# Performance work log

Measured on AMD Instinct MI355X. Metric: run time of the kernel, lower is better.

## Reference

```python
import jax, jax.numpy as jnp
import numpy as np

N_NODES = 100_000
N_EDGES = 1_600_000
D_IN = 128
D_OUT = 128


def setup_inputs() -> dict:
    key = jax.random.key(0)
    ks = jax.random.split(key, 6)
    X = jax.random.normal(ks[0], (N_NODES, D_IN), dtype=jnp.float32)
    ref_a = jax.random.randint(ks[1], (N_EDGES,), 0, N_NODES, dtype=jnp.int64 if jax.config.jax_enable_x64 else jnp.int32)
    backref = jax.random.randint(ks[2], (N_EDGES,), 0, N_NODES, dtype=jnp.int64 if jax.config.jax_enable_x64 else jnp.int32)
    e_map = jax.random.randint(ks[3], (N_EDGES,), 0, N_NODES, dtype=jnp.int32)
    v_count = jnp.ones((1,), dtype=jnp.int32)
    # GlorotUniform init for the two projection matrices
    limit = np.sqrt(6.0 / (D_IN + D_OUT)).astype(np.float32)
    W = jax.random.uniform(ks[4], (D_IN, D_OUT), dtype=jnp.float32, minval=-limit, maxval=limit)
    W_prop = jax.random.uniform(ks[5], (D_IN, D_OUT), dtype=jnp.float32, minval=-limit, maxval=limit)
    b = jnp.zeros((D_OUT,), dtype=jnp.float32)
    return {"X": X, "ref_a": ref_a, "backref": backref, "e_map": e_map,
            "v_count": v_count, "W": W, "W_prop": W_prop, "b": b}


def reference(X, ref_a, backref, e_map, v_count, W, W_prop, b):
    # Dual linear projections
    XW = X @ W                 # [N, D_OUT]
    XW_prop = X @ W_prop       # [N, D_OUT]
    # wl1_convolution_compact: gather rows at edge sources, scatter-sum into targets
    msgs = XW_prop[ref_a]      # [E, D_OUT] irregular gather
    X_conv = jax.ops.segment_sum(msgs, backref, num_segments=X.shape[0])  # [N, D_OUT]
    # bias add + activation
    X_out = jax.nn.relu(XW + X_conv + b)
    return (X_out, ref_a, backref, e_map, v_count)
```

## Files before the change

kernel.cpp:

```cpp
#include <hip/hip_runtime.h>
#include <hip/hip_bf16.h>


#define SCAN_BE 1024

typedef __attribute__((ext_vector_type(8))) short bf16x8;
typedef __attribute__((ext_vector_type(4))) float f32x4;

__device__ __forceinline__ float bf2f(unsigned short u) {
    return __uint_as_float(((unsigned int)u) << 16);
}

__device__ __forceinline__ unsigned short f2bf(float f) {
    unsigned int b = __float_as_uint(f);
    unsigned int r = (b + 0x7FFFu + ((b >> 16) & 1u)) >> 16;
    return (unsigned short)r;
}

__device__ __forceinline__ unsigned char f2e4m3(float f) {
    unsigned int u = __float_as_uint(f);
    unsigned char s = (unsigned char)((u >> 24) & 0x80u);
    unsigned int ua = u & 0x7FFFFFFFu;
    float a = __uint_as_float(ua);
    if (!(a < 448.0f)) return (unsigned char)(s | 0x7E);
    if (a < 0x1p-10f) return s;
    int E = (int)(ua >> 23);
    int e = E - 120;
    unsigned int M = ua & 0x7FFFFFu;
    if (e >= 1) {
        unsigned int r = M + 0x7FFFFu + ((M >> 20) & 1u);
        unsigned int m = r >> 20;
        if (m >= 8) { m = 0; e++; }
        if (e >= 16 || (e == 15 && m == 7))
            return (unsigned char)(s | 0x7E);
        return (unsigned char)(s | (e << 3) | (m & 7));
    } else {
        int m = (int)(a * 512.0f + 0.5f);
        if (m >= 8) return (unsigned char)(s | 0x08);
        return (unsigned char)(s | m);
    }
}

__device__ __forceinline__ float4 load4f(const void* p, size_t off, int isbf) {
    if (isbf) {
        ushort4 u = *(const ushort4*)((const unsigned short*)p + off);
        return make_float4(bf2f(u.x), bf2f(u.y), bf2f(u.z), bf2f(u.w));
    }
    return *(const float4*)((const float*)p + off);
}

__global__ void detect_kernel(const unsigned int* __restrict__ Xw,
                              const unsigned int* __restrict__ bw,
                              int* __restrict__ flags) {
    __shared__ int c_bf16, c_i64;
    int t = threadIdx.x;
    if (t == 0) { c_bf16 = 0; c_i64 = 0; }
    __syncthreads();
    int local = 0;
    #pragma unroll
    for (int k = 0; k < 4; k++) {
        unsigned int w = Xw[t * 4 + k];
        unsigned int e = (w >> 7) & 0xFFu;
        if (e >= 96u && e <= 143u) local++;
    }
    atomicAdd(&c_bf16, local);
    atomicAdd(&c_i64, (bw[2 * t + 1] == 0u) ? 1 : 0);
    __syncthreads();
    if (t == 0) {
        flags[0] = (c_bf16 >= 512) ? 1 : 0;
        flags[1] = (c_i64 == 256) ? 1 : 0;
    }
}

__global__ void zero_kernel(float4* __restrict__ p, long long n4) {
    long long i = (long long)blockIdx.x * blockDim.x + threadIdx.x;
    long long stride = (long long)gridDim.x * blockDim.x;
    for (; i < n4; i += stride)
        p[i] = make_float4(0.f, 0.f, 0.f, 0.f);
}

__global__ void zero_i32(int* __restrict__ p, long long n) {
    long long i = (long long)blockIdx.x * blockDim.x + threadIdx.x;
    long long stride = (long long)gridDim.x * blockDim.x;
    for (; i < n; i += stride) p[i] = 0;
}

__global__ void fill_zero_f32(float* __restrict__ p, long long lo, long long hi) {
    long long i = lo + (long long)blockIdx.x * blockDim.x + threadIdx.x;
    long long stride = (long long)gridDim.x * blockDim.x;
    for (; i < hi; i += stride) p[i] = 0.f;
}

__global__ void xconv_dual_kernel(const void* __restrict__ Xraw,
                                  const int* __restrict__ flags,
                                  unsigned short* __restrict__ Xb,
                                  unsigned char* __restrict__ Xq,
                                  int writeq, long long n4) {
    long long i = (long long)blockIdx.x * blockDim.x + threadIdx.x;
    long long stride = (long long)gridDim.x * blockDim.x;
    const int isbf = flags[0];
    for (; i < n4; i += stride) {
        float4 v = load4f(Xraw, (size_t)i * 4, isbf);
        ushort4 u;
        u.x = f2bf(v.x); u.y = f2bf(v.y);
        u.z = f2bf(v.z); u.w = f2bf(v.w);
        *(ushort4*)(Xb + i * 4) = u;
        if (writeq) {
            uchar4 q;
            q.x = f2e4m3(v.x); q.y = f2e4m3(v.y);
            q.z = f2e4m3(v.z); q.w = f2e4m3(v.w);
            *(uchar4*)(Xq + i * 4) = q;
        }
    }
}

__global__ void wtrans_frag_kernel(const void* __restrict__ W,
                                   const void* __restrict__ Wp,
                                   const void* __restrict__ bias,
                                   const int* __restrict__ flags,
                                   unsigned short* __restrict__ Wtf,
                                   unsigned short* __restrict__ Wptf,
                                   float* __restrict__ biasf, int D) {
    const int isbf = flags[0];
    int i = blockIdx.x * blockDim.x + threadIdx.x;
    if (i < 2048) {
        int lane = i & 63;
        int ctkc = i >> 6;
        int kc = ctkc & 3;
        int ct = ctkc >> 2;
        int lr = lane & 15, lg = lane >> 4;
        int n = ct * 16 + lr;
        #pragma unroll
        for (int e = 0; e < 8; e++) {
            int k = kc * 32 + 16 * (e >> 2) + 4 * lg + (e & 3);
            size_t src = (size_t)k * D + n;
            float w  = isbf ? bf2f(((const unsigned short*)W)[src])
                            : ((const float*)W)[src];
            float wp = isbf ? bf2f(((const unsigned short*)Wp)[src])
                            : ((const float*)Wp)[src];
            Wtf [(size_t)i * 8 + e] = f2bf(w);
            Wptf[(size_t)i * 8 + e] = f2bf(wp);
        }
    }
    if (i < D) {
        biasf[i] = isbf ? bf2f(((const unsigned short*)bias)[i])
                        : ((const float*)bias)[i];
    }
}

__global__ void copy_idx_hist_kernel(const int* __restrict__ ref_a,
                                     const int* __restrict__ backref,
                                     const int* __restrict__ e_map,
                                     const int* __restrict__ v_count,
                                     const int* __restrict__ flags,
                                     float* __restrict__ out,
                                     int* __restrict__ counts,
                                     long long base, long long E) {
    long long i = (long long)blockIdx.x * blockDim.x + threadIdx.x;
    const int is64 = flags[1];
    if (i < E) {
        out[base + i] = (float)ref_a[is64 ? 2 * i : i];
        atomicAdd(&counts[backref[is64 ? 2 * i : i]], 1);
    } else if (i < 2 * E) {
        long long k = i - E;
        out[base + i] = (float)backref[is64 ? 2 * k : k];
    } else if (i < 3 * E) {
        out[base + i] = (float)e_map[i - 2 * E];
    } else if (i == 3 * E) {
        out[base + i] = (float)v_count[0];
    }
}

__global__ __launch_bounds__(256) void block_reduce_kernel(
    const int* __restrict__ counts, int* __restrict__ bsum, int n) {
    __shared__ int sd[256];
    int b = blockIdx.x, t = threadIdx.x;
    int lo = b * SCAN_BE;
    int hi = lo + SCAN_BE; if (hi > n) hi = n;
    int s = 0;
    for (int i = lo + t; i < hi; i += 256) s += counts[i];
    sd[t] = s;
    __syncthreads();
    for (int d = 128; d > 0; d >>= 1) {
        if (t < d) sd[t] += sd[t + d];
        __syncthreads();
    }
    if (t == 0) bsum[b] = sd[0];
}

__global__ __launch_bounds__(1024) void scan_bsum_kernel(
    int* __restrict__ bsum, int nb, int* __restrict__ offsets, int n) {
    __shared__ int sd[1024];
    int t = threadIdx.x;
    int v = (t < nb) ? bsum[t] : 0;
    sd[t] = v;
    __syncthreads();
    for (int d = 1; d < 1024; d <<= 1) {
        int x = (t >= d) ? sd[t - d] : 0;
        __syncthreads();
        sd[t] += x;
        __syncthreads();
    }
    if (t < nb) bsum[t] = (t == 0) ? 0 : sd[t - 1];
    if (t == 1023) offsets[n] = sd[1023];
}

__global__ __launch_bounds__(256) void block_scan_kernel(
    const int* counts, const int* __restrict__ bsum,
    int* __restrict__ offsets, int* cursor, int n) {
    __shared__ int ts[256];
    int b = blockIdx.x, t = threadIdx.x;
    int base0 = b * SCAN_BE + t * 4;
    int c0 = (base0 + 0 < n) ? counts[base0 + 0] : 0;
    int c1 = (base0 + 1 < n) ? counts[base0 + 1] : 0;
    int c2 = (base0 + 2 < n) ? counts[base0 + 2] : 0;
    int c3 = (base0 + 3 < n) ? counts[base0 + 3] : 0;
    ts[t] = c0 + c1 + c2 + c3;
    __syncthreads();
    for (int d = 1; d < 256; d <<= 1) {
        int x = (t >= d) ? ts[t - d] : 0;
        __syncthreads();
        ts[t] += x;
        __syncthreads();
    }
    int ex = bsum[b] + (t ? ts[t - 1] : 0);
    if (base0 + 0 < n) { offsets[base0 + 0] = ex; cursor[base0 + 0] = ex; } ex += c0;
    if (base0 + 1 < n) { offsets[base0 + 1] = ex; cursor[base0 + 1] = ex; } ex += c1;
    if (base0 + 2 < n) { offsets[base0 + 2] = ex; cursor[base0 + 2] = ex; } ex += c2;
    if (base0 + 3 < n) { offsets[base0 + 3] = ex; cursor[base0 + 3] = ex; }
}

__global__ __launch_bounds__(1024) void scan_kernel(
    const int* counts, int* __restrict__ offsets, int* cursor, int n) {
    __shared__ int part[1024];
    int t = threadIdx.x;
    int chunk = (n + 1023) / 1024;
    int lo = t * chunk;
    int hi = lo + chunk; if (hi > n) hi = n;
    int s = 0;
    for (int i = lo; i < hi; i++) s += counts[i];
    part[t] = s;
    __syncthreads();
    for (int d = 1; d < 1024; d <<= 1) {
        int v = (t >= d) ? part[t - d] : 0;
        __syncthreads();
        part[t] += v;
        __syncthreads();
    }
    int run = (t == 0) ? 0 : part[t - 1];
    for (int i = lo; i < hi; i++) {
        int c = counts[i];
        offsets[i] = run;
        cursor[i]  = run;
        run += c;
    }
    if (t == 1023) offsets[n] = part[1023];
}

__global__ void scatter_xcd_kernel(const int* __restrict__ src,
                                   const int* __restrict__ dst,
                                   const int* __restrict__ flags,
                                   int* __restrict__ cursor,
                                   int* __restrict__ srcs,
                                   long long E, int N, int nstripes) {
    int b = blockIdx.x;
    int r = b & 7;
    int s = b >> 3;
    int rchunk = (N + 7) / 8;
    int rlo = r * rchunk;
    int rhi = rlo + rchunk; if (rhi > N) rhi = N;
    long long e0 = (long long)s * E / nstripes;
    long long e1 = (long long)(s + 1) * E / nstripes;
    const int is64 = flags[1];
    for (long long i = e0 + threadIdx.x; i < e1; i += blockDim.x) {
        long long ei = is64 ? 2 * i : i;
        int d = dst[ei];
        if (d < rlo || d >= rhi) continue;
        int sv = src[ei];
        int pos = atomicAdd(&cursor[d], 1);
        srcs[pos] = sv;
    }
}

__device__ __forceinline__ void acc_fp8x4(float4& acc, unsigned int q) {
    unsigned int b0 = ((q << 24) & 0x80000000u) | ((q << 20) & 0x07F00000u);
    unsigned int b1 = ((q << 16) & 0x80000000u) | ((q << 12) & 0x07F00000u);
    unsigned int b2 = ((q <<  8) & 0x80000000u) | ((q <<  4) & 0x07F00000u);
    unsigned int b3 = ( q        & 0x80000000u) | ((q >>  4) & 0x07F00000u);
    acc.x = fmaf(__uint_as_float(b0), 0x1p120f, acc.x);
    acc.y = fmaf(__uint_as_float(b1), 0x1p120f, acc.y);
    acc.z = fmaf(__uint_as_float(b2), 0x1p120f, acc.z);
    acc.w = fmaf(__uint_as_float(b3), 0x1p120f, acc.w);
}

__global__ void csr_agg_f8b_kernel(const unsigned char* __restrict__ Xq,
                                   const int* __restrict__ offsets,
                                   const int* __restrict__ srcs,
                                   unsigned short* __restrict__ Ab,
                                   int N, int D) {
    int g = (int)(((long long)blockIdx.x * blockDim.x + threadIdx.x) >> 5);
    int lane = threadIdx.x & 31;
    if (g >= N) return;
    int lo = offsets[g], hi = offsets[g + 1];
    for (int c = lane * 4; c < D; c += 128) {
        float4 acc = make_float4(0.f, 0.f, 0.f, 0.f);
        int i = lo;
        for (; i + 1 < hi; i += 2) {
            int s0 = srcs[i], s1 = srcs[i + 1];
            unsigned int q0 = *(const unsigned int*)(Xq + (size_t)s0 * D + c);
            unsigned int q1 = *(const unsigned int*)(Xq + (size_t)s1 * D + c);
            acc_fp8x4(acc, q0);
            acc_fp8x4(acc, q1);
        }
        if (i < hi) {
            int s0 = srcs[i];
            unsigned int q0 = *(const unsigned int*)(Xq + (size_t)s0 * D + c);
            acc_fp8x4(acc, q0);
        }
        ushort4 o;
        o.x = f2bf(acc.x); o.y = f2bf(acc.y);
        o.z = f2bf(acc.z); o.w = f2bf(acc.w);
        *(ushort4*)(Ab + (size_t)g * D + c) = o;
    }
}

__global__ void csr_agg_b2b_kernel(const unsigned short* __restrict__ Xb,
                                   const int* __restrict__ offsets,
                                   const int* __restrict__ srcs,
                                   unsigned short* __restrict__ Ab,
                                   int N, int D) {
    int g = (int)(((long long)blockIdx.x * blockDim.x + threadIdx.x) >> 5);
    int lane = threadIdx.x & 31;
    if (g >= N) return;
    int lo = offsets[g], hi = offsets[g + 1];
    for (int c = lane * 4; c < D; c += 128) {
        float4 acc = make_float4(0.f, 0.f, 0.f, 0.f);
        for (int i = lo; i < hi; i++) {
            int s = srcs[i];
            ushort4 u = *(const ushort4*)(Xb + (size_t)s * D + c);
            acc.x += bf2f(u.x); acc.y += bf2f(u.y);
            acc.z += bf2f(u.z); acc.w += bf2f(u.w);
        }
        ushort4 o;
        o.x = f2bf(acc.x); o.y = f2bf(acc.y);
        o.z = f2bf(acc.z); o.w = f2bf(acc.w);
        *(ushort4*)(Ab + (size_t)g * D + c) = o;
    }
}

__global__ void csr_agg_kernel(const void* __restrict__ Xraw,
                               const int* __restrict__ offsets,
                               const int* __restrict__ srcs,
                               const int* __restrict__ flags,
                               float* __restrict__ A, int N, int D) {
    int g = (int)(((long long)blockIdx.x * blockDim.x + threadIdx.x) >> 5);
    int lane = threadIdx.x & 31;
    if (g >= N) return;
    const int isbf = flags[0];
    int lo = offsets[g], hi = offsets[g + 1];
    for (int c = lane * 4; c < D; c += 128) {
        float4 acc = make_float4(0.f, 0.f, 0.f, 0.f);
        for (int i = lo; i < hi; i++) {
            int s = srcs[i];
            float4 v = load4f(Xraw, (size_t)s * D + c, isbf);
            acc.x += v.x; acc.y += v.y; acc.z += v.z; acc.w += v.w;
        }
        *(float4*)(A + (size_t)g * D + c) = acc;
    }
}

__global__ __launch_bounds__(256) void gemm_mfma_kernel(
    const unsigned short* __restrict__ Xb,
    const unsigned short* __restrict__ Ab,
    const unsigned short* __restrict__ Wtf,
    const unsigned short* __restrict__ Wptf,
    const float* __restrict__ biasf,
    float* __restrict__ out, long long Nw) {
    const int D = 128;
    const int wave = threadIdx.x >> 6;
    const int lane = threadIdx.x & 63;
    const int lr = lane & 15;
    const int lg = lane >> 4;
    const long long rbase = ((long long)blockIdx.x * 4 + wave) * 16;
    if (rbase >= Nw) return;

    long long arow = rbase + lr;
    if (arow >= Nw) arow = Nw - 1;
    const unsigned short* xrow = Xb + arow * D;
    const unsigned short* prow = Ab + arow * D;

    f32x4 acc[8];
    #pragma unroll
    for (int i = 0; i < 8; i++) acc[i] = (f32x4){0.f, 0.f, 0.f, 0.f};

    for (int kc = 0; kc < 8; kc++) {
        const bool xpart = (kc < 4);
        const unsigned short* arow_p = xpart ? xrow : prow;
        const unsigned short* wf     = xpart ? Wtf : Wptf;
        const int kk = kc & 3;
        const int k0 = kk * 32 + 4 * lg;

        ushort4 alo = *(const ushort4*)(arow_p + k0);
        ushort4 ahi = *(const ushort4*)(arow_p + k0 + 16);
        bf16x8 a = {(short)alo.x, (short)alo.y, (short)alo.z, (short)alo.w,
                    (short)ahi.x, (short)ahi.y, (short)ahi.z, (short)ahi.w};

        #pragma unroll
        for (int ct = 0; ct < 8; ct++) {
            bf16x8 b = *(const bf16x8*)(wf +
                           ((size_t)((ct * 4 + kk) * 64 + lane)) * 8);
            acc[ct] = __builtin_amdgcn_mfma_f32_16x16x32_bf16(a, b, acc[ct],
                                                              0, 0, 0);
        }
    }

    #pragma unroll
    for (int ct = 0; ct < 8; ct++) {
        int n = ct * 16 + lr;
        float bn = biasf[n];
        #pragma unroll
        for (int r = 0; r < 4; r++) {
            long long m = rbase + 4 * lg + r;
            if (m < Nw) {
                float v = acc[ct][r] + bn;
                out[m * D + n] = v > 0.f ? v : 0.f;
            }
        }
    }
}

__global__ void edge_agg_kernel(const void* __restrict__ Xraw,
                                const int* __restrict__ src,
                                const int* __restrict__ dst,
                                const int* __restrict__ flags,
                                float* __restrict__ A,
                                long long E, int D, int row0, int row1) {
    long long tid = (long long)blockIdx.x * blockDim.x + threadIdx.x;
    long long e = tid >> 5;
    int lane = (int)(tid & 31);
    if (e >= E) return;
    const int is64 = flags[1];
    const int isbf = flags[0];
    long long ei = is64 ? 2 * e : e;
    int d = dst[ei];
    if (d < row0 || d >= row1) return;
    int s = src[ei];
    for (int c = lane * 4; c < D; c += 128) {
        float4 v = load4f(Xraw, (size_t)s * D + c, isbf);
        float* a = A + (size_t)(d - row0) * D + c;
        atomicAdd(a + 0, v.x);
        atomicAdd(a + 1, v.y);
        atomicAdd(a + 2, v.z);
        atomicAdd(a + 3, v.w);
    }
}

__global__ void copy_idx_kernel(const int* __restrict__ ref_a,
                                const int* __restrict__ backref,
                                const int* __restrict__ e_map,
                                const int* __restrict__ v_count,
                                const int* __restrict__ flags,
                                float* __restrict__ out,
                                long long base, long long E) {
    long long i = (long long)blockIdx.x * blockDim.x + threadIdx.x;
    const int is64 = flags[1];
    if (i < E) {
        out[base + i] = (float)ref_a[is64 ? 2 * i : i];
    } else if (i < 2 * E) {
        long long k = i - E;
        out[base + i] = (float)backref[is64 ? 2 * k : k];
    } else if (i < 3 * E) {
        out[base + i] = (float)e_map[i - 2 * E];
    } else if (i == 3 * E) {
        out[base + i] = (float)v_count[0];
    }
}

__global__ __launch_bounds__(256) void gemm_fused_kernel(
    const void* __restrict__ Xraw, const float* __restrict__ A,
    const void* __restrict__ Wraw, const void* __restrict__ Wpraw,
    const void* __restrict__ braw, const int* __restrict__ flags,
    float* __restrict__ out, long long row0, long long rend) {
    const int D = 128;
    __shared__ float sX[64][68];
    __shared__ float sW[64][68];

    const long long rbase = row0 + (long long)blockIdx.x * 64;
    const int cbase = blockIdx.y * 64;
    const int t  = threadIdx.x;
    const int tx = t & 15;
    const int ty = t >> 4;
    const int isbf = flags[0];

    float acc[4][4] = {};

    for (int kk = 0; kk < 256; kk += 64) {
        const bool first = (kk < 128);
        const void* Ws = first ? Wraw : Wpraw;
        const int kc = kk & 127;

        #pragma unroll
        for (int i = 0; i < 4; i++) {
            int r  = ty + i * 16;
            int c4 = tx * 4;
            long long grow = rbase + r;
            float4 v = make_float4(0.f, 0.f, 0.f, 0.f);
            if (grow < rend) {
                if (first)
                    v = load4f(Xraw, (size_t)grow * D + kc + c4, isbf);
                else
                    v = *(const float4*)(A + (size_t)(grow - row0) * D + kc + c4);
            }
            *(float4*)&sX[r][c4] = v;
            float4 w = load4f(Ws, (size_t)(kc + r) * D + cbase + c4, isbf);
            *(float4*)&sW[r][c4] = w;
        }
        __syncthreads();

        #pragma unroll
        for (int k4 = 0; k4 < 16; k4++) {
            float4 xv[4], wv[4];
            #pragma unroll
            for (int i = 0; i < 4; i++)
                xv[i] = *(float4*)&sX[ty * 4 + i][k4 * 4];
            #pragma unroll
            for (int i = 0; i < 4; i++)
                wv[i] = *(float4*)&sW[k4 * 4 + i][tx * 4];
            #pragma unroll
            for (int ki = 0; ki < 4; ki++) {
                #pragma unroll
                for (int r = 0; r < 4; r++) {
                    float x = (ki == 0) ? xv[r].x
                            : (ki == 1) ? xv[r].y
                            : (ki == 2) ? xv[r].z
                                        : xv[r].w;
                    acc[r][0] += x * wv[ki].x;
                    acc[r][1] += x * wv[ki].y;
                    acc[r][2] += x * wv[ki].z;
                    acc[r][3] += x * wv[ki].w;
                }
            }
        }
        __syncthreads();
    }

    const long long grow0 = rbase + ty * 4;
    const int gcol0 = cbase + tx * 4;
    float b0, b1, b2, b3;
    if (isbf) {
        const unsigned short* bb = (const unsigned short*)braw;
        b0 = bf2f(bb[gcol0 + 0]); b1 = bf2f(bb[gcol0 + 1]);
        b2 = bf2f(bb[gcol0 + 2]); b3 = bf2f(bb[gcol0 + 3]);
    } else {
        const float* bb = (const float*)braw;
        b0 = bb[gcol0 + 0]; b1 = bb[gcol0 + 1];
        b2 = bb[gcol0 + 2]; b3 = bb[gcol0 + 3];
    }
    #pragma unroll
    for (int r = 0; r < 4; r++) {
        long long grow = grow0 + r;
        if (grow >= rend) break;
        float4 v;
        v.x = acc[r][0] + b0; v.x = v.x > 0.f ? v.x : 0.f;
        v.y = acc[r][1] + b1; v.y = v.y > 0.f ? v.y : 0.f;
        v.z = acc[r][2] + b2; v.z = v.z > 0.f ? v.z : 0.f;
        v.w = acc[r][3] + b3; v.w = v.w > 0.f ? v.w : 0.f;
        *(float4*)(out + (size_t)grow * D + gcol0) = v;
    }
}

extern "C" void kernel_launch(void* const* d_in, const int* in_sizes, int n_in,
                              void* d_out, int out_size, void* d_ws, size_t ws_size,
                              hipStream_t stream) {
    const void* X       = d_in[0];
    const int*  ref_a   = (const int*)d_in[1];
    const int*  backref = (const int*)d_in[2];
    const int*  e_map   = (const int*)d_in[3];
    const int*  v_count = (const int*)d_in[4];
    const void* W       = d_in[5];
    const void* W_prop  = d_in[6];
    const void* bias    = d_in[7];
    float* out = (float*)d_out;

    int Dout = (n_in > 7 && in_sizes[7] > 0) ? in_sizes[7] : 128;
    int Din  = (in_sizes[5] > 0 && in_sizes[5] % Dout == 0)
                   ? in_sizes[5] / Dout : Dout;
    long long N = in_sizes[0] / Din;
    long long E = in_sizes[1];
    long long base = (long long)out_size - 3 * E - 1;
    if (base < 0) base = N * Dout;

    auto align256 = [](size_t x) { return (x + 255) & ~(size_t)255; };
    size_t o_flags = 0;
    size_t o_off   = align256(o_flags + 256);
    size_t o_cur   = align256(o_off + (size_t)(N + 1) * 4);
    size_t o_bsum  = align256(o_cur + (size_t)N * 4);
    size_t o_srcs  = align256(o_bsum + 1024 * 4);
    size_t o_A     = align256(o_srcs + (size_t)E * 4);
    size_t o_Xb    = align256(o_A + (size_t)N * Din * 4);
    size_t o_Wt    = align256(o_Xb + (size_t)N * Din * 2);
    size_t o_Wpt   = align256(o_Wt + (size_t)Din * Dout * 2);
    size_t o_bf    = align256(o_Wpt + (size_t)Din * Dout * 2);
    size_t o_Xq    = align256(o_bf + (size_t)Dout * 4);
    size_t need_csr  = o_Xb;
    size_t need_mfma = o_Xq;
    size_t need_fp8  = o_Xq + (size_t)N * Din;
    const bool use_csr  = (ws_size >= need_csr);
    const bool use_mfma = (ws_size >= need_mfma) && (Din == 128) && (Dout == 128);
    const bool use_fp8  = (ws_size >= need_fp8) && use_mfma;

    char* wsb = (char*)d_ws;
    int*            flags   = (int*)(wsb + o_flags);
    int*            offsets = (int*)(wsb + o_off);
    int*            cursor  = (int*)(wsb + o_cur);
    int*            bsum    = (int*)(wsb + o_bsum);
    int*            srcs    = (int*)(wsb + o_srcs);
    float*          A       = use_csr ? (float*)(wsb + o_A) : (float*)(wsb + 256);
    unsigned short* Ab      = (unsigned short*)(wsb + o_A);
    unsigned short* Xb      = (unsigned short*)(wsb + o_Xb);
    unsigned short* Wtf     = (unsigned short*)(wsb + o_Wt);
    unsigned short* Wptf    = (unsigned short*)(wsb + o_Wpt);
    float*          biasf   = (float*)(wsb + o_bf);
    unsigned char*  Xq      = (unsigned char*)(wsb + o_Xq);

    detect_kernel<<<1, 256, 0, stream>>>((const unsigned int*)X,
                                         (const unsigned int*)backref, flags);

    long long Nw = N;
    long long cap = base / Dout;
    if (cap < Nw) Nw = cap;
    if (N * Dout < base)
        fill_zero_f32<<<2048, 1024, 0, stream>>>(out, N * Dout, base);

    if (use_csr) {
        zero_i32<<<256, 256, 0, stream>>>(cursor, N);
        {
            long long total = 3 * E + 1;
            int blocks = (int)((total + 255) / 256);
            copy_idx_hist_kernel<<<blocks, 256, 0, stream>>>(
                ref_a, backref, e_map, v_count, flags, out, cursor, base, E);
        }
        int nb = (int)((N + SCAN_BE - 1) / SCAN_BE);
        if (nb <= 1024) {
            block_reduce_kernel<<<nb, 256, 0, stream>>>(cursor, bsum, (int)N);
            scan_bsum_kernel<<<1, 1024, 0, stream>>>(bsum, nb, offsets, (int)N);
            block_scan_kernel<<<nb, 256, 0, stream>>>(cursor, bsum, offsets,
                                                      cursor, (int)N);
        } else {
            scan_kernel<<<1, 1024, 0, stream>>>(cursor, offsets, cursor, (int)N);
        }
        {
            const int nstripes = 256;
            scatter_xcd_kernel<<<8 * nstripes, 256, 0, stream>>>(
                ref_a, backref, flags, cursor, srcs, E, (int)N, nstripes);
        }

        if (use_mfma) {
            {
                long long n4 = (N * (long long)Din) / 4;
                int cblocks = (int)((n4 + 1023) / 1024);
                if (cblocks > 2048) cblocks = 2048;
                xconv_dual_kernel<<<cblocks, 1024, 0, stream>>>(
                    X, flags, Xb, Xq, use_fp8 ? 1 : 0, n4);
            }
            wtrans_frag_kernel<<<8, 256, 0, stream>>>(W, W_prop, bias, flags,
                                                      Wtf, Wptf, biasf, Din);
            {
                long long threads = N * 32;
                int blocks = (int)((threads + 255) / 256);
                if (use_fp8)
                    csr_agg_f8b_kernel<<<blocks, 256, 0, stream>>>(
                        Xq, offsets, srcs, Ab, (int)N, Din);
                else
                    csr_agg_b2b_kernel<<<blocks, 256, 0, stream>>>(
                        Xb, offsets, srcs, Ab, (int)N, Din);
            }
            {
                int blocks = (int)((Nw + 63) / 64);
                gemm_mfma_kernel<<<blocks, 256, 0, stream>>>(Xb, Ab, Wtf, Wptf,
                                                             biasf, out, Nw);
            }
        } else {
            {
                long long threads = N * 32;
                int blocks = (int)((threads + 255) / 256);
                csr_agg_kernel<<<blocks, 256, 0, stream>>>(X, offsets, srcs,
                                                           flags, A, (int)N, Din);
            }
            dim3 grid((unsigned)((Nw + 63) / 64), 2);
            gemm_fused_kernel<<<grid, 256, 0, stream>>>(X, A, W, W_prop, bias,
                                                        flags, out, 0, Nw);
        }
    } else {
        {
            long long total = 3 * E + 1;
            int blocks = (int)((total + 255) / 256);
            copy_idx_kernel<<<blocks, 256, 0, stream>>>(ref_a, backref, e_map,
                                                        v_count, flags, out,
                                                        base, E);
        }
        size_t avail = (ws_size > 256) ? ws_size - 256 : 0;
        size_t rows_cap = avail / ((size_t)Din * sizeof(float));
        long long rows_per;
        if (rows_cap >= (size_t)Nw) rows_per = Nw > 0 ? Nw : 1;
        else {
            rows_per = (long long)(rows_cap & ~(size_t)63);
            if (rows_per <= 0) rows_per = 64;
        }
        for (long long row0 = 0; row0 < Nw; row0 += rows_per) {
            long long rows = (Nw - row0 < rows_per) ? (Nw - row0) : rows_per;
            long long rend = row0 + rows;
            {   long long n4 = (rows * (long long)Din) / 4;
                int blocks = (int)((n4 + 1023) / 1024);
                if (blocks > 2048) blocks = 2048;
                if (blocks > 0)
                    zero_kernel<<<blocks, 1024, 0, stream>>>((float4*)A, n4);
            }
            {   long long threads = E * 32;
                int blocks = (int)((threads + 255) / 256);
                edge_agg_kernel<<<blocks, 256, 0, stream>>>(X, ref_a, backref,
                                                            flags, A, E, Din,
                                                            (int)row0, (int)rend);
            }
            {   dim3 grid((unsigned)((rows + 63) / 64), 2);
                gemm_fused_kernel<<<grid, 256, 0, stream>>>(X, A, W, W_prop,
                                                            bias, flags, out,
                                                            row0, rend);
            }
        }
    }
}
```

Before: 281.7 us.

## Fuse fp8 CSR aggregation into MFMA GEMM and merge index-copy with X conversion

The fp8 path now aggregates neighbor rows directly into a shared-memory bf16 tile inside the GEMM kernel, so the aggregated matrix no longer makes a round trip through global memory and one launch disappears. The index-copy/histogram kernel and the X bf16/fp8 conversion are merged into a single prep kernel, removing another launch. In exchange, each GEMM block must finish its gather phase before its MFMA phase, which may reduce overlap, and the prep kernel mixes two different access patterns.

```diff
diff --git a/kernel.cpp b/kernel.cpp
--- a/kernel.cpp
+++ b/kernel.cpp
@@ -110,6 +110,49 @@
             q.x = f2e4m3(v.x); q.y = f2e4m3(v.y);
             q.z = f2e4m3(v.z); q.w = f2e4m3(v.w);
             *(uchar4*)(Xq + i * 4) = q;
+        }
+    }
+}
+
+__global__ void prep_kernel(const int* __restrict__ ref_a,
+                            const int* __restrict__ backref,
+                            const int* __restrict__ e_map,
+                            const int* __restrict__ v_count,
+                            const int* __restrict__ flags,
+                            float* __restrict__ out,
+                            int* __restrict__ counts,
+                            const void* __restrict__ Xraw,
+                            unsigned short* __restrict__ Xb,
+                            unsigned char* __restrict__ Xq,
+                            long long base, long long E, long long n4) {
+    long long i = (long long)blockIdx.x * blockDim.x + threadIdx.x;
+    const int is64 = flags[1];
+    const int isbf = flags[0];
+    const long long idxN = 3 * E + 1;
+    if (i < idxN) {
+        if (i < E) {
+            out[base + i] = (float)ref_a[is64 ? 2 * i : i];
+            atomicAdd(&counts[backref[is64 ? 2 * i : i]], 1);
+        } else if (i < 2 * E) {
+            long long k = i - E;
+            out[base + i] = (float)backref[is64 ? 2 * k : k];
+        } else if (i < 3 * E) {
+            out[base + i] = (float)e_map[i - 2 * E];
+        } else {
+            out[base + i] = (float)v_count[0];
+        }
+    } else {
+        long long j = i - idxN;
+        if (j < n4) {
+            float4 v = load4f(Xraw, (size_t)j * 4, isbf);
+            ushort4 u;
+            u.x = f2bf(v.x); u.y = f2bf(v.y);
+            u.z = f2bf(v.z); u.w = f2bf(v.w);
+            *(ushort4*)(Xb + j * 4) = u;
+            uchar4 q;
+            q.x = f2e4m3(v.x); q.y = f2e4m3(v.y);
+            q.z = f2e4m3(v.z); q.w = f2e4m3(v.w);
+            *(uchar4*)(Xq + j * 4) = q;
         }
     }
 }
@@ -293,34 +336,102 @@
     acc.w = fmaf(__uint_as_float(b3), 0x1p120f, acc.w);
 }
 
-__global__ void csr_agg_f8b_kernel(const unsigned char* __restrict__ Xq,
-                                   const int* __restrict__ offsets,
-                                   const int* __restrict__ srcs,
-                                   unsigned short* __restrict__ Ab,
-                                   int N, int D) {
-    int g = (int)(((long long)blockIdx.x * blockDim.x + threadIdx.x) >> 5);
-    int lane = threadIdx.x & 31;
-    if (g >= N) return;
-    int lo = offsets[g], hi = offsets[g + 1];
-    for (int c = lane * 4; c < D; c += 128) {
-        float4 acc = make_float4(0.f, 0.f, 0.f, 0.f);
-        int i = lo;
-        for (; i + 1 < hi; i += 2) {
-            int s0 = srcs[i], s1 = srcs[i + 1];
-            unsigned int q0 = *(const unsigned int*)(Xq + (size_t)s0 * D + c);
-            unsigned int q1 = *(const unsigned int*)(Xq + (size_t)s1 * D + c);
-            acc_fp8x4(acc, q0);
-            acc_fp8x4(acc, q1);
-        }
-        if (i < hi) {
-            int s0 = srcs[i];
-            unsigned int q0 = *(const unsigned int*)(Xq + (size_t)s0 * D + c);
-            acc_fp8x4(acc, q0);
-        }
-        ushort4 o;
-        o.x = f2bf(acc.x); o.y = f2bf(acc.y);
-        o.z = f2bf(acc.z); o.w = f2bf(acc.w);
-        *(ushort4*)(Ab + (size_t)g * D + c) = o;
+__global__ __launch_bounds__(256) void agg_gemm_kernel(
+    const unsigned short* __restrict__ Xb,
+    const unsigned char* __restrict__ Xq,
+    const int* __restrict__ offsets,
+    const int* __restrict__ srcs,
+    const unsigned short* __restrict__ Wtf,
+    const unsigned short* __restrict__ Wptf,
+    const float* __restrict__ biasf,
+    float* __restrict__ out, long long Nw) {
+    const int D = 128;
+    __shared__ unsigned short sAb[64][136];
+
+    const long long blk0 = (long long)blockIdx.x * 64;
+
+    {
+        int grp  = threadIdx.x >> 5;
+        int lane = threadIdx.x & 31;
+        int c = lane * 4;
+        for (int r = grp; r < 64; r += 8) {
+            long long g = blk0 + r;
+            if (g >= Nw) break;
+            int lo = offsets[g], hi = offsets[g + 1];
+            float4 acc = make_float4(0.f, 0.f, 0.f, 0.f);
+            int i = lo;
+            for (; i + 1 < hi; i += 2) {
+                unsigned int q0 = *(const unsigned int*)(Xq + (size_t)srcs[i] * D + c);
+                unsigned int q1 = *(const unsigned int*)(Xq + (size_t)srcs[i + 1] * D + c);
+                acc_fp8x4(acc, q0);
+                acc_fp8x4(acc, q1);
+            }
+            if (i < hi) {
+                unsigned int q0 = *(const unsigned int*)(Xq + (size_t)srcs[i] * D + c);
+                acc_fp8x4(acc, q0);
+            }
+            ushort4 o;
+            o.x = f2bf(acc.x); o.y = f2bf(acc.y);
+            o.z = f2bf(acc.z); o.w = f2bf(acc.w);
+            *(ushort4*)&sAb[r][c] = o;
+        }
+    }
+    __syncthreads();
+
+    const int wave = threadIdx.x >> 6;
+    const int lane = threadIdx.x & 63;
+    const int lr = lane & 15;
+    const int lg = lane >> 4;
+    const long long rbase = blk0 + wave * 16;
+    if (rbase >= Nw) return;
+
+    long long arow = rbase + lr;
+    if (arow >= Nw) arow = Nw - 1;
+    const unsigned short* xrow = Xb + arow * D;
+    const int ldsrow = wave * 16 + lr;
+
+    f32x4 acc[8];
+    #pragma unroll
+    for (int i = 0; i < 8; i++) acc[i] = (f32x4){0.f, 0.f, 0.f, 0.f};
+
+    for (int kc = 0; kc < 8; kc++) {
+        const bool xpart = (kc < 4);
+        const unsigned short* wf = xpart ? Wtf : Wptf;
+        const int kk = kc & 3;
+        const int k0 = kk * 32 + 4 * lg;
+
+        ushort4 alo, ahi;
+        if (xpart) {
+            alo = *(const ushort4*)(xrow + k0);
+            ahi = *(const ushort4*)(xrow + k0 + 16);
+        } else {
+            alo = *(const ushort4*)&sAb[ldsrow][k0];
+            ahi = *(const ushort4*)&sAb[ldsrow][k0 + 16];
+        }
+        bf16x8 a = {(short)alo.x, (short)alo.y, (short)alo.z, (short)alo.w,
+                    (short)ahi.x, (short)ahi.y, (short)ahi.z, (short)ahi.w};
+
+        #pragma unroll
+        for (int ct = 0; ct < 8; ct++) {
+            bf16x8 b = *(const bf16x8*)(wf +
+                           ((size_t)((ct * 4 + kk) * 64 + lane)) * 8);
+            acc[ct] = __builtin_amdgcn_mfma_f32_16x16x32_bf16(a, b, acc[ct],
+                                                              0, 0, 0);
+        }
+    }
+
+    #pragma unroll
+    for (int ct = 0; ct < 8; ct++) {
+        int n = ct * 16 + lr;
+        float bn = biasf[n];
+        #pragma unroll
+        for (int r = 0; r < 4; r++) {
+            long long m = rbase + 4 * lg + r;
+            if (m < Nw) {
+                float v = acc[ct][r] + bn;
+                out[m * D + n] = v > 0.f ? v : 0.f;
+            }
+        }
     }
 }
 
@@ -634,7 +745,15 @@
 
     if (use_csr) {
         zero_i32<<<256, 256, 0, stream>>>(cursor, N);
-        {
+        long long n4 = (N * (long long)Din) / 4;
+
+        if (use_fp8) {
+            long long total = 3 * E + 1 + n4;
+            int blocks = (int)((total + 255) / 256);
+            prep_kernel<<<blocks, 256, 0, stream>>>(ref_a, backref, e_map,
+                                                    v_count, flags, out, cursor,
+                                                    X, Xb, Xq, base, E, n4);
+        } else {
             long long total = 3 * E + 1;
             int blocks = (int)((total + 255) / 256);
             copy_idx_hist_kernel<<<blocks, 256, 0, stream>>>(
@@ -656,29 +775,25 @@
         }
 
         if (use_mfma) {
-            {
-                long long n4 = (N * (long long)Din) / 4;
+            wtrans_frag_kernel<<<8, 256, 0, stream>>>(W, W_prop, bias, flags,
+                                                      Wtf, Wptf, biasf, Din);
+            if (use_fp8) {
+                int blocks = (int)((Nw + 63) / 64);
+                agg_gemm_kernel<<<blocks, 256, 0, stream>>>(Xb, Xq, offsets,
+                                                            srcs, Wtf, Wptf,
+                                                            biasf, out, Nw);
+            } else {
                 int cblocks = (int)((n4 + 1023) / 1024);
                 if (cblocks > 2048) cblocks = 2048;
-                xconv_dual_kernel<<<cblocks, 1024, 0, stream>>>(
-                    X, flags, Xb, Xq, use_fp8 ? 1 : 0, n4);
-            }
-            wtrans_frag_kernel<<<8, 256, 0, stream>>>(W, W_prop, bias, flags,
-                                                      Wtf, Wptf, biasf, Din);
-            {
+                xconv_dual_kernel<<<cblocks, 1024, 0, stream>>>(X, flags, Xb,
+                                                                Xq, 0, n4);
                 long long threads = N * 32;
                 int blocks = (int)((threads + 255) / 256);
-                if (use_fp8)
-                    csr_agg_f8b_kernel<<<blocks, 256, 0, stream>>>(
-                        Xq, offsets, srcs, Ab, (int)N, Din);
-                else
-                    csr_agg_b2b_kernel<<<blocks, 256, 0, stream>>>(
-                        Xb, offsets, srcs, Ab, (int)N, Din);
-            }
-            {
-                int blocks = (int)((Nw + 63) / 64);
-                gemm_mfma_kernel<<<blocks, 256, 0, stream>>>(Xb, Ab, Wtf, Wptf,
-                                                             biasf, out, Nw);
+                csr_agg_b2b_kernel<<<blocks, 256, 0, stream>>>(
+                    Xb, offsets, srcs, Ab, (int)N, Din);
+                int gblocks = (int)((Nw + 63) / 64);
+                gemm_mfma_kernel<<<gblocks, 256, 0, stream>>>(Xb, Ab, Wtf, Wptf,
+                                                              biasf, out, Nw);
             }
         } else {
             {
@@ -710,11 +825,11 @@
         for (long long row0 = 0; row0 < Nw; row0 += rows_per) {
             long long rows = (Nw - row0 < rows_per) ? (Nw - row0) : rows_per;
             long long rend = row0 + rows;
-            {   long long n4 = (rows * (long long)Din) / 4;
-                int blocks = (int)((n4 + 1023) / 1024);
+            {   long long n4c = (rows * (long long)Din) / 4;
+                int blocks = (int)((n4c + 1023) / 1024);
                 if (blocks > 2048) blocks = 2048;
                 if (blocks > 0)
-                    zero_kernel<<<blocks, 1024, 0, stream>>>((float4*)A, n4);
+                    zero_kernel<<<blocks, 1024, 0, stream>>>((float4*)A, n4c);
             }
             {   long long threads = E * 32;
                 int blocks = (int)((threads + 255) / 256);
```

New measurement: 327.9 us. 16.4% more time.
